# Performance work log

Hardware: AMD Instinct MI355X
Metric: run time of the kernel (lower is better)

Reference implementation:

```python
import jax, jax.numpy as jnp
from jax import lax
import numpy as np

R = 256            # reservoir_size
LUT_LEN = 18       # 2**18 LUT entries per node
B = 8              # bits_per_feature
D = 4              # n_features
M = 512            # samples
S = 512            # steps
OUT = 10           # output_size


def _first_primes(n):
    sieve = np.ones(2000, dtype=bool)
    sieve[:2] = False
    for i in range(2, 45):
        if sieve[i]:
            sieve[i * i::i] = False
    return np.nonzero(sieve)[0][:n].astype(np.int32)


def setup_inputs() -> dict:
    key = jax.random.key(0)
    ks = jax.random.split(key, 7)
    x = jax.random.randint(ks[0], (M, S, D, B), 0, 2).astype(bool)
    lut = jax.random.randint(ks[1], (R, 2 ** LUT_LEN), 0, 2).astype(jnp.int32)
    init_res = jax.random.randint(ks[2], (R,), 0, 2).astype(bool)
    W_res = jax.random.randint(ks[3], (R, R), 0, 2).astype(bool)
    input_nodes = jax.random.permutation(ks[4], R)[: B * D].astype(jnp.int32)
    primes = jnp.asarray(_first_primes(R))
    readout_W = jax.random.normal(ks[5], (OUT, R), dtype=jnp.float32) * (1.0 / np.sqrt(R))
    readout_b = jax.random.normal(ks[6], (OUT,), dtype=jnp.float32) * 0.01
    return {
        "x": x,
        "input_nodes": input_nodes,
        "lut": lut,
        "W_res": W_res,
        "primes": primes,
        "init_res": init_res,
        "readout_W": readout_W,
        "readout_b": readout_b,
    }


def _run_reservoir(x, input_nodes, lut, W_res, primes, init_res):
    m, s, d, b = x.shape
    xf = x.reshape(m, s, d * b).astype(jnp.int32)          # [m, s, d*b]
    # row j of Wp holds primes[k] * W_res[j, k]; idx = r @ Wp.T
    Wp = W_res.astype(jnp.int32) * primes[None, :]          # [R, R]
    node_idx = jnp.arange(R)[None, :]                       # [1, R]
    r0 = jnp.broadcast_to(init_res.astype(jnp.int32), (m, R))

    def step(r, x_t):
        # write encoded input bits into the reservoir, then LUT-perturb
        r = r.at[:, input_nodes].set(x_t)                   # [m, R]
        idx = r @ Wp.T                                      # [m, R] state indices
        r_new = jnp.take_along_axis(lut[None].repeat(1, 0)[0][node_idx.repeat(m, 0) * 0 + node_idx, idx], jnp.zeros((m, R, 1), jnp.int32), axis=-1) if False else lut[node_idx, idx]
        return r_new.astype(jnp.int32), None

    rf, _ = lax.scan(step, r0, jnp.swapaxes(xf, 0, 1))      # scan over s steps
    return rf                                               # [m, R] final states (0/1)


def reference(x, input_nodes, lut, W_res, primes, init_res, readout_W, readout_b):
    rf = _run_reservoir(x, input_nodes, lut, W_res, primes, init_res)
    return rf.astype(jnp.float32) @ readout_W.T + readout_b  # [m, output_size]
```

## Files before the change

### kernel.cpp

```cpp
#include <hip/hip_runtime.h>
#include <stdint.h>

#define R_NODES 256
#define M_SAMP  512
#define S_STEPS 512
#define OUT_N   10

__global__ void detect_layout(const uint8_t* __restrict__ x, int* __restrict__ flag) {
    __shared__ int any;
    if (threadIdx.x == 0) any = 0;
    __syncthreads();
    int acc = 0;
    for (int i = 0; i < 64; ++i)
        acc |= x[(size_t)(threadIdx.x * 64 + i) * 4 + 1];
    if (acc) atomicOr(&any, 1);
    __syncthreads();
    if (threadIdx.x == 0) *flag = any ? 1 : 0;
}

__global__ void pack_x(const uint8_t* __restrict__ x, const int* __restrict__ flag,
                       uint32_t* __restrict__ xp) {
    const int stride = (*flag) ? 1 : 4;
    const int f = blockIdx.x * blockDim.x + threadIdx.x;
    const int val = x[(size_t)f * stride];
    const uint64_t mask = __ballot(val != 0);
    const int lane = threadIdx.x & 63;
    if ((lane & 31) == 0) {
        uint32_t w = (lane & 32) ? (uint32_t)(mask >> 32) : (uint32_t)mask;
        xp[f >> 5] = w;
    }
}

__global__ void build_T2(const uint8_t* __restrict__ wres, const int* __restrict__ primes,
                         const int* __restrict__ flag, uint16_t* __restrict__ T2) {
    const int v = blockIdx.x;
    const int c = blockIdx.y;
    const int j = threadIdx.x;
    const int stride = (*flag) ? 1 : 4;
    int sum = 0;
#pragma unroll
    for (int b = 0; b < 8; ++b) {
        if ((v >> b) & 1) {
            const int k = c * 8 + b;
            if (wres[(size_t)(j * 256 + k) * stride]) sum += primes[k];
        }
    }
    T2[((size_t)v * 32 + c) * 256 + j] = (uint16_t)sum;
}

__device__ __forceinline__ uint32_t spread8(uint32_t x) {
    x = (x | (x << 12)) & 0x000F000Fu;
    x = (x | (x << 6))  & 0x03030303u;
    x = (x | (x << 3))  & 0x11111111u;
    return x;
}
__global__ void pack_lut(const int* __restrict__ lut, uint32_t* __restrict__ lp32) {
    const int lane = threadIdx.x & 63;
    const int gw = blockIdx.x * (blockDim.x >> 6) + (threadIdx.x >> 6);
    const int4* src = (const int4*)lut;
    for (int it = 0; it < 128; ++it) {
        const int chunk = gw * 128 + it;
        const int4 q = src[(size_t)chunk * 64 + lane];
        const uint64_t b0 = __ballot((q.x & 1) != 0);
        const uint64_t b1 = __ballot((q.y & 1) != 0);
        const uint64_t b2 = __ballot((q.z & 1) != 0);
        const uint64_t b3 = __ballot((q.w & 1) != 0);
        if (lane < 8) {
            const uint32_t B0 = (uint32_t)(b0 >> (8 * lane)) & 0xFF;
            const uint32_t B1 = (uint32_t)(b1 >> (8 * lane)) & 0xFF;
            const uint32_t B2 = (uint32_t)(b2 >> (8 * lane)) & 0xFF;
            const uint32_t B3 = (uint32_t)(b3 >> (8 * lane)) & 0xFF;
            const uint32_t w = spread8(B0) | (spread8(B1) << 1)
                             | (spread8(B2) << 2) | (spread8(B3) << 3);
            lp32[(size_t)chunk * 8 + lane] = w;
        }
    }
}

__global__ __launch_bounds__(256, 2) void reservoir_main(
    const uint32_t* __restrict__ xp, const uint16_t* __restrict__ T2,
    const uint64_t* __restrict__ lp, const int* __restrict__ input_nodes,
    const uint8_t* __restrict__ init_res, const int* __restrict__ flag,
    const float* __restrict__ rW, const float* __restrict__ rb,
    float* __restrict__ out)
{
    const int m = blockIdx.x;
    const int t = threadIdx.x;
    const int wid = t >> 6;
    const int lane = t & 63;
    const int rg = t >> 5;
    const int cg = t & 31;
    __shared__ uint64_t lmask[4];
    __shared__ uint16_t part[8][256];
    __shared__ float lout[OUT_N];

    const int stride = (*flag) ? 1 : 4;
    int slot = -1;
#pragma unroll
    for (int i = 0; i < 32; ++i)
        if (input_nodes[i] == t) slot = i;

    int v = init_res[(size_t)t * stride] ? 1 : 0;
    const uint64_t* lrow = lp + (size_t)t * 4096;
    const uint32_t* xrow = xp + m * S_STEPS;

    for (int s = 0; s < S_STEPS; ++s) {
        const uint32_t xw = xrow[s];
        if (slot >= 0) v = (xw >> slot) & 1;
        const uint64_t bal = __ballot(v != 0);
        if (lane == 0) lmask[wid] = bal;
        __syncthreads();
        const uint64_t mw = lmask[rg >> 1];
        const uint32_t half = (uint32_t)(mw >> ((rg & 1) * 32));
        const int c0 = rg * 4;
        const uint4* a0 = (const uint4*)(T2 + (size_t)(((int)( half        & 0xFF) * 32 + c0 + 0) * 256)) + cg;
        const uint4* a1 = (const uint4*)(T2 + (size_t)(((int)((half >>  8) & 0xFF) * 32 + c0 + 1) * 256)) + cg;
        const uint4* a2 = (const uint4*)(T2 + (size_t)(((int)((half >> 16) & 0xFF) * 32 + c0 + 2) * 256)) + cg;
        const uint4* a3 = (const uint4*)(T2 + (size_t)(((int)( half >> 24        ) * 32 + c0 + 3) * 256)) + cg;
        const uint4 l0 = *a0;
        const uint4 l1 = *a1;
        const uint4 l2 = *a2;
        const uint4 l3 = *a3;
        uint4 sm;
        sm.x = l0.x + l1.x + l2.x + l3.x;
        sm.y = l0.y + l1.y + l2.y + l3.y;
        sm.z = l0.z + l1.z + l2.z + l3.z;
        sm.w = l0.w + l1.w + l2.w + l3.w;
        *(uint4*)&part[rg][cg * 8] = sm;
        __syncthreads();
        int idx = 0;
#pragma unroll
        for (int r = 0; r < 8; ++r) idx += part[r][t];
        v = (int)((lrow[idx >> 6] >> (idx & 63)) & 1);
    }

    __syncthreads();
    if (t < OUT_N) lout[t] = 0.f;
    __syncthreads();
#pragma unroll
    for (int o = 0; o < OUT_N; ++o) {
        float contrib = v ? rW[o * R_NODES + t] : 0.f;
        for (int off = 32; off > 0; off >>= 1)
            contrib += __shfl_down(contrib, off, 64);
        if (lane == 0) atomicAdd(&lout[o], contrib);
    }
    __syncthreads();
    if (t < OUT_N) out[m * OUT_N + t] = lout[t] + rb[t];
}

extern "C" void kernel_launch(void* const* d_in, const int* in_sizes, int n_in,
                              void* d_out, int out_size, void* d_ws, size_t ws_size,
                              hipStream_t stream) {
    const uint8_t* x        = (const uint8_t*)d_in[0];
    const int* input_nodes  = (const int*)d_in[1];
    const int* lut          = (const int*)d_in[2];
    const uint8_t* wres     = (const uint8_t*)d_in[3];
    const int* primes       = (const int*)d_in[4];
    const uint8_t* init_res = (const uint8_t*)d_in[5];
    const float* rW         = (const float*)d_in[6];
    const float* rb         = (const float*)d_in[7];
    float* out              = (float*)d_out;

    uint8_t* ws = (uint8_t*)d_ws;
    int*      flag = (int*)ws;
    uint32_t* xp   = (uint32_t*)(ws + 4096);
    uint16_t* T2   = (uint16_t*)(ws + 4096 + 1048576);
    uint64_t* lp   = (uint64_t*)(ws + 4096 + 1048576 + 4194304);

    detect_layout<<<1, 256, 0, stream>>>(x, flag);
    pack_x<<<(M_SAMP * S_STEPS * 32) / 256, 256, 0, stream>>>(x, flag, xp);
    build_T2<<<dim3(256, 32), 256, 0, stream>>>(wres, primes, flag, T2);
    pack_lut<<<512, 256, 0, stream>>>(lut, (uint32_t*)lp);
    reservoir_main<<<M_SAMP, 256, 0, stream>>>(xp, T2, lp, input_nodes, init_res,
                                               flag, rW, rb, out);
}
```

Baseline: 999.0 us.

## Run each sample's reservoir in a single wavefront with no block barriers

The main kernel moves from a 256-thread block, which needed two __syncthreads and a shared-memory partial-sum reduction every step, to one 64-lane wavefront per sample. Each lane now owns four nodes. State bits are gathered with ballots and readlane, and the T2 byte-table index is remapped (bit order permuted in build_T2) so each lane reads a contiguous uint2 holding its four 16-bit partial sums. The LUT packing launch is also spread over more blocks for parallelism. In exchange each step does 32 serialized table loads per lane and occupancy drops to 512 single-wave blocks.

```diff
diff --git a/kernel.cpp b/kernel.cpp
--- a/kernel.cpp
+++ b/kernel.cpp
@@ -39,9 +39,9 @@
     const int stride = (*flag) ? 1 : 4;
     int sum = 0;
 #pragma unroll
-    for (int b = 0; b < 8; ++b) {
-        if ((v >> b) & 1) {
-            const int k = c * 8 + b;
+    for (int p = 0; p < 8; ++p) {
+        if ((v >> p) & 1) {
+            const int k = c * 8 + ((p & 1) << 2) + (p >> 1);
             if (wres[(size_t)(j * 256 + k) * stride]) sum += primes[k];
         }
     }
@@ -58,8 +58,8 @@
     const int lane = threadIdx.x & 63;
     const int gw = blockIdx.x * (blockDim.x >> 6) + (threadIdx.x >> 6);
     const int4* src = (const int4*)lut;
-    for (int it = 0; it < 128; ++it) {
-        const int chunk = gw * 128 + it;
+    for (int it = 0; it < 16; ++it) {
+        const int chunk = gw * 16 + it;
         const int4 q = src[(size_t)chunk * 64 + lane];
         const uint64_t b0 = __ballot((q.x & 1) != 0);
         const uint64_t b1 = __ballot((q.y & 1) != 0);
@@ -77,7 +77,7 @@
     }
 }
 
-__global__ __launch_bounds__(256, 2) void reservoir_main(
+__global__ __launch_bounds__(64, 1) void reservoir_wave(
     const uint32_t* __restrict__ xp, const uint16_t* __restrict__ T2,
     const uint64_t* __restrict__ lp, const int* __restrict__ input_nodes,
     const uint8_t* __restrict__ init_res, const int* __restrict__ flag,
@@ -85,67 +85,82 @@
     float* __restrict__ out)
 {
     const int m = blockIdx.x;
-    const int t = threadIdx.x;
-    const int wid = t >> 6;
-    const int lane = t & 63;
-    const int rg = t >> 5;
-    const int cg = t & 31;
-    __shared__ uint64_t lmask[4];
-    __shared__ uint16_t part[8][256];
-    __shared__ float lout[OUT_N];
+    const int l = threadIdx.x;
+    const int stride = (*flag) ? 1 : 4;
 
-    const int stride = (*flag) ? 1 : 4;
-    int slot = -1;
-#pragma unroll
-    for (int i = 0; i < 32; ++i)
-        if (input_nodes[i] == t) slot = i;
+    int slot0 = -1, slot1 = -1, slot2 = -1, slot3 = -1;
+    for (int i = 0; i < 32; ++i) {
+        const int n = input_nodes[i];
+        if (n == 4 * l + 0) slot0 = i;
+        if (n == 4 * l + 1) slot1 = i;
+        if (n == 4 * l + 2) slot2 = i;
+        if (n == 4 * l + 3) slot3 = i;
+    }
+    int v0 = init_res[(size_t)(4 * l + 0) * stride] ? 1 : 0;
+    int v1 = init_res[(size_t)(4 * l + 1) * stride] ? 1 : 0;
+    int v2 = init_res[(size_t)(4 * l + 2) * stride] ? 1 : 0;
+    int v3 = init_res[(size_t)(4 * l + 3) * stride] ? 1 : 0;
 
-    int v = init_res[(size_t)t * stride] ? 1 : 0;
-    const uint64_t* lrow = lp + (size_t)t * 4096;
     const uint32_t* xrow = xp + m * S_STEPS;
+    const uint16_t* T2l  = T2 + 4 * l;
 
     for (int s = 0; s < S_STEPS; ++s) {
         const uint32_t xw = xrow[s];
-        if (slot >= 0) v = (xw >> slot) & 1;
-        const uint64_t bal = __ballot(v != 0);
-        if (lane == 0) lmask[wid] = bal;
-        __syncthreads();
-        const uint64_t mw = lmask[rg >> 1];
-        const uint32_t half = (uint32_t)(mw >> ((rg & 1) * 32));
-        const int c0 = rg * 4;
-        const uint4* a0 = (const uint4*)(T2 + (size_t)(((int)( half        & 0xFF) * 32 + c0 + 0) * 256)) + cg;
-        const uint4* a1 = (const uint4*)(T2 + (size_t)(((int)((half >>  8) & 0xFF) * 32 + c0 + 1) * 256)) + cg;
-        const uint4* a2 = (const uint4*)(T2 + (size_t)(((int)((half >> 16) & 0xFF) * 32 + c0 + 2) * 256)) + cg;
-        const uint4* a3 = (const uint4*)(T2 + (size_t)(((int)( half >> 24        ) * 32 + c0 + 3) * 256)) + cg;
-        const uint4 l0 = *a0;
-        const uint4 l1 = *a1;
-        const uint4 l2 = *a2;
-        const uint4 l3 = *a3;
-        uint4 sm;
-        sm.x = l0.x + l1.x + l2.x + l3.x;
-        sm.y = l0.y + l1.y + l2.y + l3.y;
-        sm.z = l0.z + l1.z + l2.z + l3.z;
-        sm.w = l0.w + l1.w + l2.w + l3.w;
-        *(uint4*)&part[rg][cg * 8] = sm;
-        __syncthreads();
-        int idx = 0;
+        if (slot0 >= 0) v0 = (xw >> slot0) & 1;
+        if (slot1 >= 0) v1 = (xw >> slot1) & 1;
+        if (slot2 >= 0) v2 = (xw >> slot2) & 1;
+        if (slot3 >= 0) v3 = (xw >> slot3) & 1;
+
+        const uint64_t b0 = __ballot(v0 != 0);
+        const uint64_t b1 = __ballot(v1 != 0);
+        const uint64_t b2 = __ballot(v2 != 0);
+        const uint64_t b3 = __ballot(v3 != 0);
+
+        const int sh = (2 * l) & 63;
+        const uint32_t u = (((uint32_t)(b0 >> sh) & 3u))
+                         | (((uint32_t)(b1 >> sh) & 3u) << 2)
+                         | (((uint32_t)(b2 >> sh) & 3u) << 4)
+                         | (((uint32_t)(b3 >> sh) & 3u) << 6);
+
+        uint32_t i0 = 0, i1 = 0, i2 = 0, i3 = 0;
 #pragma unroll
-        for (int r = 0; r < 8; ++r) idx += part[r][t];
-        v = (int)((lrow[idx >> 6] >> (idx & 63)) & 1);
+        for (int g = 0; g < 8; ++g) {
+            uint32_t lo = 0, hi = 0;
+#pragma unroll
+            for (int cc = 0; cc < 4; ++cc) {
+                const int c = 4 * g + cc;
+                const int uc = __builtin_amdgcn_readlane((int)u, c) & 0xFF;
+                const uint2 d = *(const uint2*)(T2l + (size_t)((uc << 5) + c) * 256);
+                lo += d.x;
+                hi += d.y;
+            }
+            i0 += lo & 0xFFFFu;  i1 += lo >> 16;
+            i2 += hi & 0xFFFFu;  i3 += hi >> 16;
+        }
+
+        const uint64_t w0 = lp[((size_t)(4 * l + 0) << 12) + (i0 >> 6)];
+        const uint64_t w1 = lp[((size_t)(4 * l + 1) << 12) + (i1 >> 6)];
+        const uint64_t w2 = lp[((size_t)(4 * l + 2) << 12) + (i2 >> 6)];
+        const uint64_t w3 = lp[((size_t)(4 * l + 3) << 12) + (i3 >> 6)];
+        v0 = (int)((w0 >> (i0 & 63)) & 1);
+        v1 = (int)((w1 >> (i1 & 63)) & 1);
+        v2 = (int)((w2 >> (i2 & 63)) & 1);
+        v3 = (int)((w3 >> (i3 & 63)) & 1);
     }
 
-    __syncthreads();
-    if (t < OUT_N) lout[t] = 0.f;
-    __syncthreads();
 #pragma unroll
     for (int o = 0; o < OUT_N; ++o) {
-        float contrib = v ? rW[o * R_NODES + t] : 0.f;
+        const float* wrow = rW + o * R_NODES + 4 * l;
+        float c = 0.f;
+        if (v0) c += wrow[0];
+        if (v1) c += wrow[1];
+        if (v2) c += wrow[2];
+        if (v3) c += wrow[3];
+#pragma unroll
         for (int off = 32; off > 0; off >>= 1)
-            contrib += __shfl_down(contrib, off, 64);
-        if (lane == 0) atomicAdd(&lout[o], contrib);
+            c += __shfl_down(c, off, 64);
+        if (l == 0) out[m * OUT_N + o] = c + rb[o];
     }
-    __syncthreads();
-    if (t < OUT_N) out[m * OUT_N + t] = lout[t] + rb[t];
 }
 
 extern "C" void kernel_launch(void* const* d_in, const int* in_sizes, int n_in,
@@ -170,7 +185,7 @@
     detect_layout<<<1, 256, 0, stream>>>(x, flag);
     pack_x<<<(M_SAMP * S_STEPS * 32) / 256, 256, 0, stream>>>(x, flag, xp);
     build_T2<<<dim3(256, 32), 256, 0, stream>>>(wres, primes, flag, T2);
-    pack_lut<<<512, 256, 0, stream>>>(lut, (uint32_t*)lp);
-    reservoir_main<<<M_SAMP, 256, 0, stream>>>(xp, T2, lp, input_nodes, init_res,
-                                               flag, rW, rb, out);
+    pack_lut<<<4096, 256, 0, stream>>>(lut, (uint32_t*)lp);
+    reservoir_wave<<<M_SAMP, 64, 0, stream>>>(xp, T2, lp, input_nodes, init_res,
+                                              flag, rW, rb, out);
 }
```

Result: slower. 1.484 ms (+48.6%).

## Switch to 4-bit partial-sum table with 512-thread blocks and inline-asm loads

Applied to the files above, without the earlier changes.

Replaces the 8-bit-chunk prime-sum table (4 MB) with a 4-bit-chunk table (512 KB) so it fits better in cache. Each block now has 512 threads that do four lookups each, combined through a cross-half shuffle. The input words are staged in shared memory and the next step's word is prefetched. Table and LUT loads use inline global_load with scalar bases, and pack_lut is spread over more blocks. The costs are doubled thread count with half of them idle during the LUT lookup phase, and manual vmcnt waits that prevent overlap.

```diff
diff --git a/kernel.cpp b/kernel.cpp
--- a/kernel.cpp
+++ b/kernel.cpp
@@ -5,6 +5,9 @@
 #define M_SAMP  512
 #define S_STEPS 512
 #define OUT_N   10
+
+typedef unsigned int u32x2 __attribute__((ext_vector_type(2)));
+typedef unsigned int u32x4 __attribute__((ext_vector_type(4)));
 
 __global__ void detect_layout(const uint8_t* __restrict__ x, int* __restrict__ flag) {
     __shared__ int any;
@@ -31,21 +34,21 @@
     }
 }
 
-__global__ void build_T2(const uint8_t* __restrict__ wres, const int* __restrict__ primes,
-                         const int* __restrict__ flag, uint16_t* __restrict__ T2) {
+__global__ void build_T1(const uint8_t* __restrict__ wres, const int* __restrict__ primes,
+                         const int* __restrict__ flag, uint16_t* __restrict__ T1) {
     const int v = blockIdx.x;
     const int c = blockIdx.y;
     const int j = threadIdx.x;
     const int stride = (*flag) ? 1 : 4;
     int sum = 0;
 #pragma unroll
-    for (int b = 0; b < 8; ++b) {
-        if ((v >> b) & 1) {
-            const int k = c * 8 + b;
+    for (int p = 0; p < 4; ++p) {
+        if ((v >> p) & 1) {
+            const int k = c * 4 + p;
             if (wres[(size_t)(j * 256 + k) * stride]) sum += primes[k];
         }
     }
-    T2[((size_t)v * 32 + c) * 256 + j] = (uint16_t)sum;
+    T1[((size_t)v * 64 + c) * 256 + j] = (uint16_t)sum;
 }
 
 __device__ __forceinline__ uint32_t spread8(uint32_t x) {
@@ -58,8 +61,8 @@
     const int lane = threadIdx.x & 63;
     const int gw = blockIdx.x * (blockDim.x >> 6) + (threadIdx.x >> 6);
     const int4* src = (const int4*)lut;
-    for (int it = 0; it < 128; ++it) {
-        const int chunk = gw * 128 + it;
+    for (int it = 0; it < 16; ++it) {
+        const int chunk = gw * 16 + it;
         const int4 q = src[(size_t)chunk * 64 + lane];
         const uint64_t b0 = __ballot((q.x & 1) != 0);
         const uint64_t b1 = __ballot((q.y & 1) != 0);
@@ -77,8 +80,8 @@
     }
 }
 
-__global__ __launch_bounds__(256, 2) void reservoir_main(
-    const uint32_t* __restrict__ xp, const uint16_t* __restrict__ T2,
+__global__ __launch_bounds__(512, 1) void reservoir_block(
+    const uint32_t* __restrict__ xp, const uint16_t* __restrict__ T1,
     const uint64_t* __restrict__ lp, const int* __restrict__ input_nodes,
     const uint8_t* __restrict__ init_res, const int* __restrict__ flag,
     const float* __restrict__ rW, const float* __restrict__ rb,
@@ -86,66 +89,111 @@
 {
     const int m = blockIdx.x;
     const int t = threadIdx.x;
-    const int wid = t >> 6;
-    const int lane = t & 63;
-    const int rg = t >> 5;
-    const int cg = t & 31;
-    __shared__ uint64_t lmask[4];
+    const int l = t & 63;
+    const int w = t >> 6;
+    const int stride = (*flag) ? 1 : 4;
+
+    __shared__ uint32_t smask[8];
     __shared__ uint16_t part[8][256];
-    __shared__ float lout[OUT_N];
-
-    const int stride = (*flag) ? 1 : 4;
-    int slot = -1;
-#pragma unroll
-    for (int i = 0; i < 32; ++i)
-        if (input_nodes[i] == t) slot = i;
-
-    int v = init_res[(size_t)t * stride] ? 1 : 0;
-    const uint64_t* lrow = lp + (size_t)t * 4096;
+    __shared__ uint32_t sxw[S_STEPS];
+    __shared__ float    lout[OUT_N];
+
     const uint32_t* xrow = xp + m * S_STEPS;
+    for (int i = t; i < S_STEPS; i += 512) sxw[i] = xrow[i];
+
+    int slot = -1, v = 0;
+    if (t < 256) {
+        for (int i = 0; i < 32; ++i)
+            if (input_nodes[i] == t) slot = i;
+        v = init_res[(size_t)t * stride] ? 1 : 0;
+    }
+
+    const int cg  = t & 31;
+    const int rq  = t >> 5;
+    const int wb  = rq >> 3;
+    const int sh4 = (rq & 7) * 4;
+
+    const uint64_t t1base = (uint64_t)(uintptr_t)T1;
+    const uint64_t lpbase = (uint64_t)(uintptr_t)lp;
+    const uint32_t colb   = (uint32_t)cg << 4;
+
+    __syncthreads();
+    uint32_t xw = sxw[0];
 
     for (int s = 0; s < S_STEPS; ++s) {
-        const uint32_t xw = xrow[s];
-        if (slot >= 0) v = (xw >> slot) & 1;
-        const uint64_t bal = __ballot(v != 0);
-        if (lane == 0) lmask[wid] = bal;
+        if (t < 256) {
+            if (slot >= 0) v = (xw >> slot) & 1;
+            const uint64_t bal = __ballot(v != 0);
+            if (l == 0) {
+                smask[2 * w]     = (uint32_t)bal;
+                smask[2 * w + 1] = (uint32_t)(bal >> 32);
+            }
+        }
         __syncthreads();
-        const uint64_t mw = lmask[rg >> 1];
-        const uint32_t half = (uint32_t)(mw >> ((rg & 1) * 32));
-        const int c0 = rg * 4;
-        const uint4* a0 = (const uint4*)(T2 + (size_t)(((int)( half        & 0xFF) * 32 + c0 + 0) * 256)) + cg;
-        const uint4* a1 = (const uint4*)(T2 + (size_t)(((int)((half >>  8) & 0xFF) * 32 + c0 + 1) * 256)) + cg;
-        const uint4* a2 = (const uint4*)(T2 + (size_t)(((int)((half >> 16) & 0xFF) * 32 + c0 + 2) * 256)) + cg;
-        const uint4* a3 = (const uint4*)(T2 + (size_t)(((int)( half >> 24        ) * 32 + c0 + 3) * 256)) + cg;
-        const uint4 l0 = *a0;
-        const uint4 l1 = *a1;
-        const uint4 l2 = *a2;
-        const uint4 l3 = *a3;
-        uint4 sm;
-        sm.x = l0.x + l1.x + l2.x + l3.x;
-        sm.y = l0.y + l1.y + l2.y + l3.y;
-        sm.z = l0.z + l1.z + l2.z + l3.z;
-        sm.w = l0.w + l1.w + l2.w + l3.w;
-        *(uint4*)&part[rg][cg * 8] = sm;
+
+        const uint32_t mw0 = smask[wb];
+        const uint32_t mw1 = smask[wb + 2];
+        const uint32_t mw2 = smask[wb + 4];
+        const uint32_t mw3 = smask[wb + 6];
+        const uint32_t o0 = (((mw0 >> sh4) & 0xFu) << 15) | ((uint32_t)(rq     ) << 9) | colb;
+        const uint32_t o1 = (((mw1 >> sh4) & 0xFu) << 15) | ((uint32_t)(rq + 16) << 9) | colb;
+        const uint32_t o2 = (((mw2 >> sh4) & 0xFu) << 15) | ((uint32_t)(rq + 32) << 9) | colb;
+        const uint32_t o3 = (((mw3 >> sh4) & 0xFu) << 15) | ((uint32_t)(rq + 48) << 9) | colb;
+        u32x4 d0, d1, d2, d3;
+        asm volatile("global_load_dwordx4 %0, %1, %2" : "=v"(d0) : "v"(o0), "s"(t1base));
+        asm volatile("global_load_dwordx4 %0, %1, %2" : "=v"(d1) : "v"(o1), "s"(t1base));
+        asm volatile("global_load_dwordx4 %0, %1, %2" : "=v"(d2) : "v"(o2), "s"(t1base));
+        asm volatile("global_load_dwordx4 %0, %1, %2" : "=v"(d3) : "v"(o3), "s"(t1base));
+        const uint32_t xw_next = sxw[(s + 1 < S_STEPS) ? s + 1 : s];
+        asm volatile("s_waitcnt vmcnt(0)");
+        asm volatile("" : "+v"(d0), "+v"(d1), "+v"(d2), "+v"(d3));
+
+        u32x4 sm;
+        sm[0] = d0[0] + d1[0] + d2[0] + d3[0];
+        sm[1] = d0[1] + d1[1] + d2[1] + d3[1];
+        sm[2] = d0[2] + d1[2] + d2[2] + d3[2];
+        sm[3] = d0[3] + d1[3] + d2[3] + d3[3];
+        sm[0] += (uint32_t)__shfl_xor((int)sm[0], 32, 64);
+        sm[1] += (uint32_t)__shfl_xor((int)sm[1], 32, 64);
+        sm[2] += (uint32_t)__shfl_xor((int)sm[2], 32, 64);
+        sm[3] += (uint32_t)__shfl_xor((int)sm[3], 32, 64);
+        if (l < 32) *(u32x4*)&part[w][cg * 8] = sm;
         __syncthreads();
-        int idx = 0;
-#pragma unroll
-        for (int r = 0; r < 8; ++r) idx += part[r][t];
-        v = (int)((lrow[idx >> 6] >> (idx & 63)) & 1);
-    }
+
+        if (t < 256) {
+            uint32_t idx = 0;
+#pragma unroll
+            for (int q = 0; q < 8; ++q) idx += (uint32_t)part[q][t];
+            u32x2 wv;
+            const uint32_t o = ((uint32_t)t << 15) + ((idx >> 6) << 3);
+            asm volatile("global_load_dwordx2 %0, %1, %2" : "=v"(wv) : "v"(o), "s"(lpbase));
+            asm volatile("s_waitcnt vmcnt(0)");
+            asm volatile("" : "+v"(wv));
+            v = (int)(((((uint64_t)wv[1] << 32) | wv[0]) >> (idx & 63)) & 1);
+        }
+        xw = xw_next;
+    }
+
+    const float* rWo;
+    const float* rbo;
+    asm volatile("" : "=s"(rWo) : "0"(rW));
+    asm volatile("" : "=s"(rbo) : "0"(rb));
 
     __syncthreads();
     if (t < OUT_N) lout[t] = 0.f;
     __syncthreads();
-#pragma unroll
-    for (int o = 0; o < OUT_N; ++o) {
-        float contrib = v ? rW[o * R_NODES + t] : 0.f;
-        for (int off = 32; off > 0; off >>= 1)
-            contrib += __shfl_down(contrib, off, 64);
-        if (lane == 0) atomicAdd(&lout[o], contrib);
-    }
-    __syncthreads();
-    if (t < OUT_N) out[m * OUT_N + t] = lout[t] + rb[t];
+    if (t < 256) {
+#pragma unroll
+        for (int o = 0; o < OUT_N; ++o) {
+            float c = v ? rWo[o * R_NODES + t] : 0.f;
+#pragma unroll
+            for (int off = 32; off > 0; off >>= 1)
+                c += __shfl_down(c, off, 64);
+            if (l == 0) atomicAdd(&lout[o], c);
+        }
+    }
+    __syncthreads();
+    if (t < OUT_N) out[m * OUT_N + t] = lout[t] + rbo[t];
 }
 
 extern "C" void kernel_launch(void* const* d_in, const int* in_sizes, int n_in,
@@ -164,13 +212,13 @@
     uint8_t* ws = (uint8_t*)d_ws;
     int*      flag = (int*)ws;
     uint32_t* xp   = (uint32_t*)(ws + 4096);
-    uint16_t* T2   = (uint16_t*)(ws + 4096 + 1048576);
-    uint64_t* lp   = (uint64_t*)(ws + 4096 + 1048576 + 4194304);
+    uint16_t* T1   = (uint16_t*)(ws + 4096 + 1048576);
+    uint64_t* lp   = (uint64_t*)(ws + 4096 + 1048576 + 524288);
 
     detect_layout<<<1, 256, 0, stream>>>(x, flag);
     pack_x<<<(M_SAMP * S_STEPS * 32) / 256, 256, 0, stream>>>(x, flag, xp);
-    build_T2<<<dim3(256, 32), 256, 0, stream>>>(wres, primes, flag, T2);
-    pack_lut<<<512, 256, 0, stream>>>(lut, (uint32_t*)lp);
-    reservoir_main<<<M_SAMP, 256, 0, stream>>>(xp, T2, lp, input_nodes, init_res,
-                                               flag, rW, rb, out);
-}
+    build_T1<<<dim3(16, 64), 256, 0, stream>>>(wres, primes, flag, T1);
+    pack_lut<<<4096, 256, 0, stream>>>(lut, (uint32_t*)lp);
+    reservoir_block<<<M_SAMP, 512, 0, stream>>>(xp, T1, lp, input_nodes, init_res,
+                                                flag, rW, rb, out);
+}
```

After: 975.0 us. -2.4%, faster.

## Replace T2 table gather with bit-sliced popcount index computation per node

Applied to the files above, without the earlier changes.

Drops the precomputed T2 partial-sum table and its global gathers. Each thread now keeps 11 bit-planes of its prime-weighted W_res row in registers and builds the LUT index from popcounts against the 256-bit reservoir mask, so each step needs one barrier instead of two. The per-sample input words are staged in shared memory, and pack_lut is relaunched with more blocks and fewer iterations per warp. In exchange each block recomputes the bit planes from W_res at startup, and the 88 register words may cut occupancy.

```diff
diff --git a/kernel.cpp b/kernel.cpp
--- a/kernel.cpp
+++ b/kernel.cpp
@@ -31,23 +31,6 @@
     }
 }
 
-__global__ void build_T2(const uint8_t* __restrict__ wres, const int* __restrict__ primes,
-                         const int* __restrict__ flag, uint16_t* __restrict__ T2) {
-    const int v = blockIdx.x;
-    const int c = blockIdx.y;
-    const int j = threadIdx.x;
-    const int stride = (*flag) ? 1 : 4;
-    int sum = 0;
-#pragma unroll
-    for (int b = 0; b < 8; ++b) {
-        if ((v >> b) & 1) {
-            const int k = c * 8 + b;
-            if (wres[(size_t)(j * 256 + k) * stride]) sum += primes[k];
-        }
-    }
-    T2[((size_t)v * 32 + c) * 256 + j] = (uint16_t)sum;
-}
-
 __device__ __forceinline__ uint32_t spread8(uint32_t x) {
     x = (x | (x << 12)) & 0x000F000Fu;
     x = (x | (x << 6))  & 0x03030303u;
@@ -58,8 +41,8 @@
     const int lane = threadIdx.x & 63;
     const int gw = blockIdx.x * (blockDim.x >> 6) + (threadIdx.x >> 6);
     const int4* src = (const int4*)lut;
-    for (int it = 0; it < 128; ++it) {
-        const int chunk = gw * 128 + it;
+    for (int it = 0; it < 16; ++it) {
+        const int chunk = gw * 16 + it;
         const int4 q = src[(size_t)chunk * 64 + lane];
         const uint64_t b0 = __ballot((q.x & 1) != 0);
         const uint64_t b1 = __ballot((q.y & 1) != 0);
@@ -77,75 +60,106 @@
     }
 }
 
-__global__ __launch_bounds__(256, 2) void reservoir_main(
-    const uint32_t* __restrict__ xp, const uint16_t* __restrict__ T2,
-    const uint64_t* __restrict__ lp, const int* __restrict__ input_nodes,
-    const uint8_t* __restrict__ init_res, const int* __restrict__ flag,
-    const float* __restrict__ rW, const float* __restrict__ rb,
-    float* __restrict__ out)
+__global__ __launch_bounds__(256, 2) void reservoir_pop(
+    const uint32_t* __restrict__ xp, const uint64_t* __restrict__ lp,
+    const int* __restrict__ input_nodes, const uint8_t* __restrict__ wres,
+    const int* __restrict__ primes, const uint8_t* __restrict__ init_res,
+    const int* __restrict__ flag, const float* __restrict__ rW,
+    const float* __restrict__ rb, float* __restrict__ out)
 {
     const int m = blockIdx.x;
-    const int t = threadIdx.x;
-    const int wid = t >> 6;
-    const int lane = t & 63;
-    const int rg = t >> 5;
-    const int cg = t & 31;
-    __shared__ uint64_t lmask[4];
-    __shared__ uint16_t part[8][256];
-    __shared__ float lout[OUT_N];
+    const int j = threadIdx.x;
+    const int l = j & 63;
+    const int w = j >> 6;
+    const int stride = (*flag) ? 1 : 4;
 
-    const int stride = (*flag) ? 1 : 4;
+    __shared__ uint32_t sxw[S_STEPS];
+    __shared__ uint32_t rmask[2][8];
+    __shared__ float    lout[OUT_N];
+
+    const uint32_t* xrow = xp + m * S_STEPS;
+    for (int i = j; i < S_STEPS; i += 256) sxw[i] = xrow[i];
+
     int slot = -1;
+    for (int i = 0; i < 32; ++i)
+        if (input_nodes[i] == j) slot = i;
+
+    uint32_t PW[11][8];
 #pragma unroll
-    for (int i = 0; i < 32; ++i)
-        if (input_nodes[i] == t) slot = i;
-
-    int v = init_res[(size_t)t * stride] ? 1 : 0;
-    const uint64_t* lrow = lp + (size_t)t * 4096;
-    const uint32_t* xrow = xp + m * S_STEPS;
-
-    for (int s = 0; s < S_STEPS; ++s) {
-        const uint32_t xw = xrow[s];
-        if (slot >= 0) v = (xw >> slot) & 1;
-        const uint64_t bal = __ballot(v != 0);
-        if (lane == 0) lmask[wid] = bal;
-        __syncthreads();
-        const uint64_t mw = lmask[rg >> 1];
-        const uint32_t half = (uint32_t)(mw >> ((rg & 1) * 32));
-        const int c0 = rg * 4;
-        const uint4* a0 = (const uint4*)(T2 + (size_t)(((int)( half        & 0xFF) * 32 + c0 + 0) * 256)) + cg;
-        const uint4* a1 = (const uint4*)(T2 + (size_t)(((int)((half >>  8) & 0xFF) * 32 + c0 + 1) * 256)) + cg;
-        const uint4* a2 = (const uint4*)(T2 + (size_t)(((int)((half >> 16) & 0xFF) * 32 + c0 + 2) * 256)) + cg;
-        const uint4* a3 = (const uint4*)(T2 + (size_t)(((int)( half >> 24        ) * 32 + c0 + 3) * 256)) + cg;
-        const uint4 l0 = *a0;
-        const uint4 l1 = *a1;
-        const uint4 l2 = *a2;
-        const uint4 l3 = *a3;
-        uint4 sm;
-        sm.x = l0.x + l1.x + l2.x + l3.x;
-        sm.y = l0.y + l1.y + l2.y + l3.y;
-        sm.z = l0.z + l1.z + l2.z + l3.z;
-        sm.w = l0.w + l1.w + l2.w + l3.w;
-        *(uint4*)&part[rg][cg * 8] = sm;
-        __syncthreads();
-        int idx = 0;
+    for (int b = 0; b < 11; ++b)
 #pragma unroll
-        for (int r = 0; r < 8; ++r) idx += part[r][t];
-        v = (int)((lrow[idx >> 6] >> (idx & 63)) & 1);
+        for (int q = 0; q < 8; ++q) PW[b][q] = 0;
+#pragma unroll
+    for (int q = 0; q < 8; ++q) {
+        for (int bit = 0; bit < 32; ++bit) {
+            const int k = 32 * q + bit;
+            const uint32_t on = wres[(size_t)(j * 256 + k) * stride] ? 1u : 0u;
+            const uint32_t p  = on * (uint32_t)primes[k];
+#pragma unroll
+            for (int b = 0; b < 11; ++b)
+                PW[b][q] |= ((p >> b) & 1u) << bit;
+        }
     }
 
     __syncthreads();
-    if (t < OUT_N) lout[t] = 0.f;
+    {
+        int bv = init_res[(size_t)j * stride] ? 1 : 0;
+        if (slot >= 0) bv = (sxw[0] >> slot) & 1;
+        const uint64_t bal = __ballot(bv != 0);
+        if (l == 0) {
+            rmask[0][2 * w]     = (uint32_t)bal;
+            rmask[0][2 * w + 1] = (uint32_t)(bal >> 32);
+        }
+    }
+    __syncthreads();
+
+    int cur = 0;
+    int v = 0;
+    for (int s = 0; s < S_STEPS; ++s) {
+        const uint32_t R0 = rmask[cur][0], R1 = rmask[cur][1],
+                       R2 = rmask[cur][2], R3 = rmask[cur][3],
+                       R4 = rmask[cur][4], R5 = rmask[cur][5],
+                       R6 = rmask[cur][6], R7 = rmask[cur][7];
+        uint32_t idx = 0;
+#pragma unroll
+        for (int b = 0; b < 11; ++b) {
+            uint32_t a;
+            a  = (uint32_t)__popc(PW[b][0] & R0);
+            a += (uint32_t)__popc(PW[b][1] & R1);
+            a += (uint32_t)__popc(PW[b][2] & R2);
+            a += (uint32_t)__popc(PW[b][3] & R3);
+            a += (uint32_t)__popc(PW[b][4] & R4);
+            a += (uint32_t)__popc(PW[b][5] & R5);
+            a += (uint32_t)__popc(PW[b][6] & R6);
+            a += (uint32_t)__popc(PW[b][7] & R7);
+            idx += a << b;
+        }
+
+        const uint64_t wv = lp[((size_t)j << 12) + (idx >> 6)];
+        v = (int)((wv >> (idx & 63)) & 1);
+
+        int wb = v;
+        if (s + 1 < S_STEPS && slot >= 0) wb = (sxw[s + 1] >> slot) & 1;
+        const uint64_t bal = __ballot(wb != 0);
+        if (l == 0) {
+            rmask[cur ^ 1][2 * w]     = (uint32_t)bal;
+            rmask[cur ^ 1][2 * w + 1] = (uint32_t)(bal >> 32);
+        }
+        __syncthreads();
+        cur ^= 1;
+    }
+
+    if (j < OUT_N) lout[j] = 0.f;
     __syncthreads();
 #pragma unroll
     for (int o = 0; o < OUT_N; ++o) {
-        float contrib = v ? rW[o * R_NODES + t] : 0.f;
+        float c = v ? rW[o * R_NODES + j] : 0.f;
         for (int off = 32; off > 0; off >>= 1)
-            contrib += __shfl_down(contrib, off, 64);
-        if (lane == 0) atomicAdd(&lout[o], contrib);
+            c += __shfl_down(c, off, 64);
+        if (l == 0) atomicAdd(&lout[o], c);
     }
     __syncthreads();
-    if (t < OUT_N) out[m * OUT_N + t] = lout[t] + rb[t];
+    if (j < OUT_N) out[m * OUT_N + j] = lout[j] + rb[j];
 }
 
 extern "C" void kernel_launch(void* const* d_in, const int* in_sizes, int n_in,
@@ -164,13 +178,12 @@
     uint8_t* ws = (uint8_t*)d_ws;
     int*      flag = (int*)ws;
     uint32_t* xp   = (uint32_t*)(ws + 4096);
-    uint16_t* T2   = (uint16_t*)(ws + 4096 + 1048576);
-    uint64_t* lp   = (uint64_t*)(ws + 4096 + 1048576 + 4194304);
+    uint64_t* lp   = (uint64_t*)(ws + 4096 + 1048576);
 
     detect_layout<<<1, 256, 0, stream>>>(x, flag);
     pack_x<<<(M_SAMP * S_STEPS * 32) / 256, 256, 0, stream>>>(x, flag, xp);
-    build_T2<<<dim3(256, 32), 256, 0, stream>>>(wres, primes, flag, T2);
-    pack_lut<<<512, 256, 0, stream>>>(lut, (uint32_t*)lp);
-    reservoir_main<<<M_SAMP, 256, 0, stream>>>(xp, T2, lp, input_nodes, init_res,
-                                               flag, rW, rb, out);
+    pack_lut<<<4096, 256, 0, stream>>>(lut, (uint32_t*)lp);
+    reservoir_pop<<<M_SAMP, 256, 0, stream>>>(xp, lp, input_nodes, wres,
+                                              primes, init_res, flag,
+                                              rW, rb, out);
 }
```

New measurement: 1.061 ms. 1.06x slower.
